# Performance work log

Hardware: AMD Instinct MI355X
Metric: run time of the kernel (lower is better)

The kernel has to match this reference:

```python
import jax, jax.numpy as jnp
import numpy as np


def setup_inputs() -> dict:
    key = jax.random.key(0)
    k0, k1, k2, k3 = jax.random.split(key, 4)
    H = 256  # hidden_dim_size
    DK = 256
    DV = 256
    hidden_states = jax.random.normal(k0, (1, 32, H, 16, 16), dtype=jnp.float32)
    # torch nn.Linear(H, dk, bias=False) computes x @ W.T; we store W.T directly as (H, dk)
    Wq = jax.random.normal(k1, (H, DK), dtype=jnp.float32) * (1.0 / np.sqrt(H))
    Wk = jax.random.normal(k2, (H, DK), dtype=jnp.float32) * (1.0 / np.sqrt(H))
    Wv = jax.random.normal(k3, (H, DV), dtype=jnp.float32) * (1.0 / np.sqrt(H))
    return {"hidden_states": hidden_states, "Wq": Wq, "Wk": Wk, "Wv": Wv}


def reference(hidden_states, Wq, Wk, Wv):
    # (b, t, c, h, w) -> (b, t, h, w, c)
    x = jnp.transpose(hidden_states, (0, 1, 3, 4, 2))
    nb, nt, nr, nc, nh = x.shape
    xf = x.reshape(-1, nh)  # (N, H) with N = b*t*h*w
    q = xf @ Wq             # (N, dk)
    k = xf @ Wk             # (N, dk)
    v = xf @ Wv             # (N, dv)
    dk = Wq.shape[1]
    scores = (q @ k.T) / jnp.sqrt(jnp.asarray(dk, dtype=q.dtype))  # (N, N)
    attn = jax.nn.softmax(scores, axis=-1) @ v                     # (N, dv)
    out = attn.reshape(nb, nt, nr, nc, -1)
    return jnp.transpose(out, (0, 1, 4, 2, 3))  # (b, t, dv, h, w)
```

## Files before the change

kernel.cpp:

```cpp
#include <hip/hip_runtime.h>
#include <stdint.h>

typedef __attribute__((ext_vector_type(8))) short bh8;
typedef __attribute__((ext_vector_type(4))) short bh4;
typedef __attribute__((ext_vector_type(4))) float f32x4;
typedef unsigned int uint32;

__device__ __forceinline__ unsigned short f2bf(float f) {
  uint32 u = __builtin_bit_cast(uint32, f);
  u += 0x7fffu + ((u >> 16) & 1u);
  return (unsigned short)(u >> 16);
}

__device__ __forceinline__ void lds_load16(const void* g, void* l) {
  auto gp = (const __attribute__((address_space(1))) uint32*)(uintptr_t)(g);
  auto lp = (__attribute__((address_space(3))) uint32*)(uintptr_t)(l);
  __builtin_amdgcn_global_load_lds(gp, lp, 16, 0, 0);
}

__global__ __launch_bounds__(256) void k_transpose(
    const float* __restrict__ hidden, const float* __restrict__ Wq,
    const float* __restrict__ Wk, const float* __restrict__ Wv,
    unsigned short* __restrict__ xb, unsigned short* __restrict__ wt) {
  int bid = blockIdx.x, c0 = blockIdx.y * 16, tid = threadIdx.x;
  const float* in; unsigned short* out; float scale = 1.0f;
  if (bid < 32) { in = hidden + (size_t)bid * 65536; out = xb + (size_t)bid * 65536; }
  else {
    int j = bid - 32;
    in = (j == 0) ? Wq : (j == 1 ? Wk : Wv);
    out = wt + (size_t)j * 65536;
    if (j == 0) scale = 0.0625f;
  }
  __shared__ uint32 lt[256 * 9];
  uint32 pk[8];
#pragma unroll
  for (int i = 0; i < 8; ++i) {
    float a = in[(size_t)(c0 + 2 * i) * 256 + tid] * scale;
    float b = in[(size_t)(c0 + 2 * i + 1) * 256 + tid] * scale;
    pk[i] = (uint32)f2bf(a) | ((uint32)f2bf(b) << 16);
  }
#pragma unroll
  for (int i = 0; i < 8; ++i) lt[tid * 9 + i] = pk[i];
  __syncthreads();
  int q2 = tid & 1;
#pragma unroll
  for (int rr = 0; rr < 2; ++rr) {
    int r = rr * 128 + (tid >> 1);
    uint4 v;
    v.x = lt[r * 9 + q2 * 4 + 0]; v.y = lt[r * 9 + q2 * 4 + 1];
    v.z = lt[r * 9 + q2 * 4 + 2]; v.w = lt[r * 9 + q2 * 4 + 3];
    *(uint4*)(out + (size_t)r * 256 + c0 + q2 * 8) = v;
  }
}

__global__ __launch_bounds__(256, 2) void k_gemm(
    const unsigned short* __restrict__ xb, const unsigned short* __restrict__ wt,
    unsigned short* __restrict__ qb, unsigned short* __restrict__ kb,
    unsigned short* __restrict__ vtb) {
  __shared__ char lds[32768];
  char* ldsA = lds; char* ldsB = lds + 16384;
  int tid = threadIdx.x, z = blockIdx.z;
  int l = tid & 63, w = tid >> 6, g = l >> 4, r15 = l & 15;
  int wr = w >> 1, wc = w & 1;
  const unsigned short *Ag, *Bg; unsigned short* out;
  int arow0, brow0; size_t ostride;
  if (z < 2) {
    Ag = xb; arow0 = blockIdx.x * 128;
    Bg = wt + (size_t)z * 65536; brow0 = blockIdx.y * 128;
    out = z ? kb : qb; ostride = 256;
  } else {
    Ag = wt + 2 * 65536; arow0 = blockIdx.y * 128;
    Bg = xb; brow0 = blockIdx.x * 128;
    out = vtb; ostride = 8192;
  }
  f32x4 acc[4][4];
#pragma unroll
  for (int i = 0; i < 4; ++i)
#pragma unroll
    for (int j = 0; j < 4; ++j) acc[i][j] = (f32x4){0.f, 0.f, 0.f, 0.f};

  for (int kk = 0; kk < 4; ++kk) {
    int c0 = kk * 64;
    __syncthreads();
#pragma unroll
    for (int p = 0; p < 4; ++p) {
      int off = p * 4096 + tid * 16;
      int row = off >> 7, ch = (off >> 4) & 7, sc = ch ^ (row & 7);
      lds_load16((const char*)Ag + ((size_t)(arow0 + row) * 256 + c0) * 2 + sc * 16, ldsA + off);
    }
#pragma unroll
    for (int p = 0; p < 4; ++p) {
      int off = p * 4096 + tid * 16;
      int row = off >> 7, ch = (off >> 4) & 7, sc = ch ^ (row & 7);
      lds_load16((const char*)Bg + ((size_t)(brow0 + row) * 256 + c0) * 2 + sc * 16, ldsB + off);
    }
    __syncthreads();
#pragma unroll
    for (int ks = 0; ks < 2; ++ks) {
      bh8 af[4], bfr[4];
#pragma unroll
      for (int i = 0; i < 4; ++i) {
        int rowa = wr * 64 + i * 16 + r15;
        af[i] = *(const bh8*)(ldsA + rowa * 128 + (((ks * 4 + g) ^ (rowa & 7)) * 16));
        int rowb = wc * 64 + i * 16 + r15;
        bfr[i] = *(const bh8*)(ldsB + rowb * 128 + (((ks * 4 + g) ^ (rowb & 7)) * 16));
      }
#pragma unroll
      for (int i = 0; i < 4; ++i)
#pragma unroll
        for (int j = 0; j < 4; ++j)
          acc[i][j] = __builtin_amdgcn_mfma_f32_16x16x32_bf16(af[i], bfr[j], acc[i][j], 0, 0, 0);
    }
  }
  __syncthreads();
#pragma unroll
  for (int i = 0; i < 4; ++i)
#pragma unroll
    for (int j = 0; j < 4; ++j)
#pragma unroll
      for (int r = 0; r < 4; ++r) {
        int rowl = wr * 64 + i * 16 + g * 4 + r;
        int coll = wc * 64 + j * 16 + r15;
        *(unsigned short*)(lds + rowl * 256 + coll * 2) = f2bf(acc[i][j][r]);
      }
  __syncthreads();
#pragma unroll
  for (int p = 0; p < 8; ++p) {
    int off = p * 4096 + tid * 16;
    int row = off >> 8, colb = off & 255;
    *(uint4*)((char*)out + ((size_t)(arow0 + row) * ostride + (size_t)brow0) * 2 + colb) =
        *(const uint4*)(lds + off);
  }
}

__global__ __launch_bounds__(512, 2) void k_attn(
    const unsigned short* __restrict__ qg, const unsigned short* __restrict__ kg,
    const unsigned short* __restrict__ vtg, float* __restrict__ Op,
    float* __restrict__ mp, float* __restrict__ lp, int S, int shift, int KS) {
  extern __shared__ char smem[];
  int tid = threadIdx.x;
  int w = tid >> 6, l = tid & 63, g = l >> 4, r15 = l & 15;
  char* Pl = smem + 131072 + w * 2176;
  int bid = blockIdx.x;
  int s = (bid >> 1) & (S - 1);
  int qb = ((bid >> (1 + shift)) << 1) | (bid & 1);
  int qrow0 = qb * 128 + w * 16;

  bh8 qf[8];
  const char* qrow = (const char*)qg + (size_t)(qrow0 + r15) * 512;
#pragma unroll
  for (int ds = 0; ds < 8; ++ds) qf[ds] = *(const bh8*)(qrow + ds * 64 + g * 16);
  asm volatile("s_waitcnt vmcnt(0)" ::: "memory");

  f32x4 o[16];
#pragma unroll
  for (int dt = 0; dt < 16; ++dt) o[dt] = (f32x4){0.f, 0.f, 0.f, 0.f};
  float m[4], ls[4];
#pragma unroll
  for (int r = 0; r < 4; ++r) { m[r] = -INFINITY; ls[r] = 0.f; }

  int nt = KS >> 6, kb0 = s * KS;

  auto stage = [&](int buf, int kvb) {
    char* Kd = smem + buf * 65536;
    char* Vd = Kd + 32768;
#pragma unroll
    for (int p = 0; p < 4; ++p) {
      int off = p * 8192 + tid * 16;
      int row = off >> 9, ch = (off >> 4) & 31;
      lds_load16((const char*)kg + (size_t)(kvb + row) * 512 + ((ch ^ (row & 7)) * 16), Kd + off);
    }
#pragma unroll
    for (int p = 0; p < 4; ++p) {
      int off = p * 8192 + tid * 16;
      int row = off >> 7, ch = (off >> 4) & 7;
      lds_load16((const char*)vtg + (size_t)row * 16384 + (size_t)kvb * 2 + ((ch ^ (row & 7)) * 16),
                 Vd + off);
    }
  };

  stage(0, kb0);

  for (int kt = 0; kt < nt; ++kt) {
    int cur = kt & 1;
    if (kt + 1 < nt) {
      stage(cur ^ 1, kb0 + (kt + 1) * 64);
      asm volatile("s_waitcnt vmcnt(8)" ::: "memory");
    } else {
      asm volatile("s_waitcnt vmcnt(0)" ::: "memory");
    }
    __builtin_amdgcn_s_barrier();
    char* Kl = smem + cur * 65536;
    char* Vl = Kl + 32768;

    f32x4 s4[4];
#pragma unroll
    for (int it = 0; it < 4; ++it) s4[it] = (f32x4){0.f, 0.f, 0.f, 0.f};
#pragma unroll
    for (int ds = 0; ds < 8; ++ds)
#pragma unroll
      for (int it = 0; it < 4; ++it) {
        int krow = it * 16 + r15;
        bh8 kf = *(const bh8*)(Kl + krow * 512 + (((ds * 4 + g) ^ (krow & 7)) * 16));
        s4[it] = __builtin_amdgcn_mfma_f32_16x16x32_bf16(qf[ds], kf, s4[it], 0, 0, 0);
      }

    float rmax[4];
#pragma unroll
    for (int r = 0; r < 4; ++r)
      rmax[r] = fmaxf(fmaxf(s4[0][r], s4[1][r]), fmaxf(s4[2][r], s4[3][r]));
#pragma unroll
    for (int d = 1; d < 16; d <<= 1)
#pragma unroll
      for (int r = 0; r < 4; ++r) rmax[r] = fmaxf(rmax[r], __shfl_xor(rmax[r], d));
    float scl[4];
#pragma unroll
    for (int r = 0; r < 4; ++r) {
      float mn = fmaxf(m[r], rmax[r]);
      scl[r] = __expf(m[r] - mn);
      m[r] = mn;
    }
    float rsum[4] = {0.f, 0.f, 0.f, 0.f};
#pragma unroll
    for (int it = 0; it < 4; ++it)
#pragma unroll
      for (int r = 0; r < 4; ++r) {
        float pv = __expf(s4[it][r] - m[r]);
        s4[it][r] = pv;
        rsum[r] += pv;
      }
#pragma unroll
    for (int d = 1; d < 16; d <<= 1)
#pragma unroll
      for (int r = 0; r < 4; ++r) rsum[r] += __shfl_xor(rsum[r], d);
    f32x4 sv = {scl[0], scl[1], scl[2], scl[3]};
#pragma unroll
    for (int r = 0; r < 4; ++r) ls[r] = ls[r] * scl[r] + rsum[r];
#pragma unroll
    for (int dt = 0; dt < 16; ++dt) o[dt] *= sv;

#pragma unroll
    for (int it = 0; it < 4; ++it)
#pragma unroll
      for (int r = 0; r < 4; ++r) {
        int prow = g * 4 + r;
        *(unsigned short*)(Pl + prow * 136 + (it * 16 + r15) * 2) = f2bf(s4[it][r]);
      }
    asm volatile("s_waitcnt lgkmcnt(0)" ::: "memory");
    bh8 pa[2];
#pragma unroll
    for (int ks = 0; ks < 2; ++ks) {
      const char* pb = Pl + r15 * 136 + ks * 64 + g * 16;
      bh4 lo = *(const bh4*)pb;
      bh4 hi = *(const bh4*)(pb + 8);
      bh8 t;
      t[0] = lo[0]; t[1] = lo[1]; t[2] = lo[2]; t[3] = lo[3];
      t[4] = hi[0]; t[5] = hi[1]; t[6] = hi[2]; t[7] = hi[3];
      pa[ks] = t;
    }
#pragma unroll
    for (int ks = 0; ks < 2; ++ks)
#pragma unroll
      for (int dt = 0; dt < 16; ++dt) {
        int vrow = dt * 16 + r15;
        bh8 vf = *(const bh8*)(Vl + vrow * 128 + (((ks * 4 + g) ^ (vrow & 7)) * 16));
        o[dt] = __builtin_amdgcn_mfma_f32_16x16x32_bf16(pa[ks], vf, o[dt], 0, 0, 0);
      }

    asm volatile("s_waitcnt lgkmcnt(0)" ::: "memory");
    __builtin_amdgcn_s_barrier();
  }

  int nrow = qrow0 + g * 4;
  float* ob = Op + ((size_t)s * 8192 + nrow) * 256 + r15;
#pragma unroll
  for (int r = 0; r < 4; ++r)
#pragma unroll
    for (int dt = 0; dt < 16; ++dt) ob[(size_t)r * 256 + dt * 16] = o[dt][r];
  if (r15 == 0) {
#pragma unroll
    for (int r = 0; r < 4; ++r) {
      mp[(size_t)s * 8192 + nrow + r] = m[r];
      lp[(size_t)s * 8192 + nrow + r] = ls[r];
    }
  }
}

__global__ __launch_bounds__(256) void k_combine(
    const float* __restrict__ Op, const float* __restrict__ mp,
    const float* __restrict__ lp, float* __restrict__ out, int S) {
  __shared__ float wsc[4 * 256];
  __shared__ float lt[32 * 257];
  int t = blockIdx.x, dc = blockIdx.y, tid = threadIdx.x;
  {
    int n = t * 256 + tid;
    float mt = -INFINITY;
#pragma unroll 4
    for (int s = 0; s < 4; ++s)
      if (s < S) mt = fmaxf(mt, mp[(size_t)s * 8192 + n]);
    float den = 0.f;
#pragma unroll 4
    for (int s = 0; s < 4; ++s)
      if (s < S) den += __expf(mp[(size_t)s * 8192 + n] - mt) * lp[(size_t)s * 8192 + n];
    float inv = 1.0f / den;
#pragma unroll 4
    for (int s = 0; s < 4; ++s)
      if (s < S) wsc[s * 256 + tid] = __expf(mp[(size_t)s * 8192 + n] - mt) * inv;
  }
  __syncthreads();
  int dl = tid & 31, pg8 = tid >> 5;
  for (int pg = 0; pg < 32; ++pg) {
    int p = pg * 8 + pg8;
    int n = t * 256 + p;
    float a = 0.f;
#pragma unroll 4
    for (int s = 0; s < 4; ++s)
      if (s < S) a += wsc[s * 256 + p] * Op[((size_t)s * 8192 + n) * 256 + dc * 32 + dl];
    lt[dl * 257 + p] = a;
  }
  __syncthreads();
  int d8 = tid >> 5, p0 = (tid & 31) * 8;
#pragma unroll
  for (int jj = 0; jj < 4; ++jj) {
    int dd = jj * 8 + d8;
    float4 v0, v1;
    v0.x = lt[dd * 257 + p0 + 0]; v0.y = lt[dd * 257 + p0 + 1];
    v0.z = lt[dd * 257 + p0 + 2]; v0.w = lt[dd * 257 + p0 + 3];
    v1.x = lt[dd * 257 + p0 + 4]; v1.y = lt[dd * 257 + p0 + 5];
    v1.z = lt[dd * 257 + p0 + 6]; v1.w = lt[dd * 257 + p0 + 7];
    float* ob = out + (size_t)t * 65536 + (size_t)(dc * 32 + dd) * 256 + p0;
    *(float4*)ob = v0;
    *(float4*)(ob + 4) = v1;
  }
}

extern "C" void kernel_launch(void* const* d_in, const int* in_sizes, int n_in,
                              void* d_out, int out_size, void* d_ws, size_t ws_size,
                              hipStream_t stream) {
  const float* hidden = (const float*)d_in[0];
  const float* Wq = (const float*)d_in[1];
  const float* Wk = (const float*)d_in[2];
  const float* Wv = (const float*)d_in[3];
  float* out = (float*)d_out;
  char* ws = (char*)d_ws;

  const size_t off_x  = 0;
  const size_t off_wt = 4ull << 20;
  const size_t off_q  = off_wt + 3ull * 131072;
  const size_t off_k  = off_q + 8192ull * 256 * 2;
  const size_t off_vt = off_k + 8192ull * 256 * 2;
  const size_t off_O  = off_vt + 8192ull * 256 * 2;

  int S = 4;
  {
    auto need = [&](int s) {
      return off_O + (size_t)s * 8192 * 256 * 4 + (size_t)s * 8192 * 4 * 2;
    };
    if (ws_size < need(4)) S = 2;
    if (ws_size < need(2)) S = 1;
  }
  size_t off_m = off_O + (size_t)S * 8192 * 256 * 4;
  size_t off_l = off_m + (size_t)S * 8192 * 4;

  unsigned short* xb  = (unsigned short*)(ws + off_x);
  unsigned short* wt  = (unsigned short*)(ws + off_wt);
  unsigned short* qb  = (unsigned short*)(ws + off_q);
  unsigned short* kb  = (unsigned short*)(ws + off_k);
  unsigned short* vtb = (unsigned short*)(ws + off_vt);
  float* Op = (float*)(ws + off_O);
  float* mp = (float*)(ws + off_m);
  float* lp = (float*)(ws + off_l);
  int shift = (S == 4) ? 2 : (S == 2 ? 1 : 0);
  int KS = 8192 / S;

  const int attn_lds = 131072 + 8 * 2176;
  hipFuncSetAttribute((const void*)k_attn, hipFuncAttributeMaxDynamicSharedMemorySize,
                      attn_lds);

  k_transpose<<<dim3(35, 16), dim3(256), 0, stream>>>(hidden, Wq, Wk, Wv, xb, wt);
  k_gemm<<<dim3(64, 2, 3), dim3(256), 0, stream>>>(xb, wt, qb, kb, vtb);
  k_attn<<<dim3(64 * S), dim3(512), attn_lds, stream>>>(qb, kb, vtb, Op, mp, lp, S, shift, KS);
  k_combine<<<dim3(32, 8), dim3(256), 0, stream>>>(Op, mp, lp, out, S);
}
```

Baseline: 173.5 us.

## Rework attention kernel to 32x32x16 MFMA with register-resident P operand

Rewrites the flash-attention kernel to use 32x32x16 bf16 MFMA with 4 waves each owning 32 query rows, computing S^T so each lane holds one query column. The P matrix is converted to bf16 with packed cvt instructions and reshuffled across lane halves with cross-lane shuffles, removing the LDS round-trip for P. Block size drops from 512 to 256 threads with one block per CU and the LDS scratch for P is removed. The larger tiles reduce LDS reads per FLOP and softmax reduction shuffles, at the cost of fewer resident waves and higher register pressure (16 q fragments plus 8 f32x16 accumulators).

```diff
diff --git a/kernel.cpp b/kernel.cpp
--- a/kernel.cpp
+++ b/kernel.cpp
@@ -2,14 +2,20 @@
 #include <stdint.h>
 
 typedef __attribute__((ext_vector_type(8))) short bh8;
-typedef __attribute__((ext_vector_type(4))) short bh4;
 typedef __attribute__((ext_vector_type(4))) float f32x4;
+typedef __attribute__((ext_vector_type(16))) float f32x16;
 typedef unsigned int uint32;
 
 __device__ __forceinline__ unsigned short f2bf(float f) {
   uint32 u = __builtin_bit_cast(uint32, f);
   u += 0x7fffu + ((u >> 16) & 1u);
   return (unsigned short)(u >> 16);
+}
+
+__device__ __forceinline__ uint32 cvtpk_bf16(float lo, float hi) {
+  uint32 r;
+  asm("v_cvt_pk_bf16_f32 %0, %1, %2" : "=v"(r) : "v"(lo), "v"(hi));
+  return r;
 }
 
 __device__ __forceinline__ void lds_load16(const void* g, void* l) {
@@ -133,31 +139,17 @@
   }
 }
 
-__global__ __launch_bounds__(512, 2) void k_attn(
+__global__ __launch_bounds__(256, 1) void k_attn(
     const unsigned short* __restrict__ qg, const unsigned short* __restrict__ kg,
     const unsigned short* __restrict__ vtg, float* __restrict__ Op,
     float* __restrict__ mp, float* __restrict__ lp, int S, int shift, int KS) {
   extern __shared__ char smem[];
   int tid = threadIdx.x;
-  int w = tid >> 6, l = tid & 63, g = l >> 4, r15 = l & 15;
-  char* Pl = smem + 131072 + w * 2176;
+  int w = tid >> 6, l = tid & 63, col = l & 31, half = l >> 5;
   int bid = blockIdx.x;
   int s = (bid >> 1) & (S - 1);
   int qb = ((bid >> (1 + shift)) << 1) | (bid & 1);
-  int qrow0 = qb * 128 + w * 16;
-
-  bh8 qf[8];
-  const char* qrow = (const char*)qg + (size_t)(qrow0 + r15) * 512;
-#pragma unroll
-  for (int ds = 0; ds < 8; ++ds) qf[ds] = *(const bh8*)(qrow + ds * 64 + g * 16);
-  asm volatile("s_waitcnt vmcnt(0)" ::: "memory");
-
-  f32x4 o[16];
-#pragma unroll
-  for (int dt = 0; dt < 16; ++dt) o[dt] = (f32x4){0.f, 0.f, 0.f, 0.f};
-  float m[4], ls[4];
-#pragma unroll
-  for (int r = 0; r < 4; ++r) { m[r] = -INFINITY; ls[r] = 0.f; }
+  int qrow0 = qb * 128 + w * 32;
 
   int nt = KS >> 6, kb0 = s * KS;
 
@@ -165,27 +157,41 @@
     char* Kd = smem + buf * 65536;
     char* Vd = Kd + 32768;
 #pragma unroll
-    for (int p = 0; p < 4; ++p) {
-      int off = p * 8192 + tid * 16;
+    for (int p = 0; p < 8; ++p) {
+      int off = p * 4096 + tid * 16;
       int row = off >> 9, ch = (off >> 4) & 31;
       lds_load16((const char*)kg + (size_t)(kvb + row) * 512 + ((ch ^ (row & 7)) * 16), Kd + off);
     }
 #pragma unroll
-    for (int p = 0; p < 4; ++p) {
-      int off = p * 8192 + tid * 16;
+    for (int p = 0; p < 8; ++p) {
+      int off = p * 4096 + tid * 16;
       int row = off >> 7, ch = (off >> 4) & 7;
       lds_load16((const char*)vtg + (size_t)row * 16384 + (size_t)kvb * 2 + ((ch ^ (row & 7)) * 16),
                  Vd + off);
     }
   };
 
+  bh8 qf[16];
+  {
+    const char* qrow = (const char*)qg + (size_t)(qrow0 + col) * 512 + half * 16;
+#pragma unroll
+    for (int t = 0; t < 16; ++t) qf[t] = *(const bh8*)(qrow + t * 32);
+  }
+
   stage(0, kb0);
+
+  f32x16 o[8];
+#pragma unroll
+  for (int dt = 0; dt < 8; ++dt)
+#pragma unroll
+    for (int i = 0; i < 16; ++i) o[dt][i] = 0.f;
+  float m = -INFINITY, ls = 0.f;
 
   for (int kt = 0; kt < nt; ++kt) {
     int cur = kt & 1;
     if (kt + 1 < nt) {
       stage(cur ^ 1, kb0 + (kt + 1) * 64);
-      asm volatile("s_waitcnt vmcnt(8)" ::: "memory");
+      asm volatile("s_waitcnt vmcnt(16)" ::: "memory");
     } else {
       asm volatile("s_waitcnt vmcnt(0)" ::: "memory");
     }
@@ -193,96 +199,89 @@
     char* Kl = smem + cur * 65536;
     char* Vl = Kl + 32768;
 
-    f32x4 s4[4];
-#pragma unroll
-    for (int it = 0; it < 4; ++it) s4[it] = (f32x4){0.f, 0.f, 0.f, 0.f};
-#pragma unroll
-    for (int ds = 0; ds < 8; ++ds)
-#pragma unroll
-      for (int it = 0; it < 4; ++it) {
-        int krow = it * 16 + r15;
-        bh8 kf = *(const bh8*)(Kl + krow * 512 + (((ds * 4 + g) ^ (krow & 7)) * 16));
-        s4[it] = __builtin_amdgcn_mfma_f32_16x16x32_bf16(qf[ds], kf, s4[it], 0, 0, 0);
+    f32x16 sc0, sc1;
+#pragma unroll
+    for (int i = 0; i < 16; ++i) { sc0[i] = 0.f; sc1[i] = 0.f; }
+#pragma unroll
+    for (int t = 0; t < 16; ++t) {
+      int r0 = col, r1 = 32 + col;
+      bh8 kf0 = *(const bh8*)(Kl + r0 * 512 + (((2 * t + half) ^ (r0 & 7)) * 16));
+      bh8 kf1 = *(const bh8*)(Kl + r1 * 512 + (((2 * t + half) ^ (r1 & 7)) * 16));
+      sc0 = __builtin_amdgcn_mfma_f32_32x32x16_bf16(kf0, qf[t], sc0, 0, 0, 0);
+      sc1 = __builtin_amdgcn_mfma_f32_32x32x16_bf16(kf1, qf[t], sc1, 0, 0, 0);
+    }
+
+    float rm = sc0[0];
+#pragma unroll
+    for (int i = 1; i < 16; ++i) rm = fmaxf(rm, sc0[i]);
+#pragma unroll
+    for (int i = 0; i < 16; ++i) rm = fmaxf(rm, sc1[i]);
+    rm = fmaxf(rm, __shfl_xor(rm, 32));
+    float mn = fmaxf(m, rm);
+    float scl = __expf(m - mn);
+    m = mn;
+    float rsum = 0.f;
+#pragma unroll
+    for (int i = 0; i < 16; ++i) { sc0[i] = __expf(sc0[i] - mn); rsum += sc0[i]; }
+#pragma unroll
+    for (int i = 0; i < 16; ++i) { sc1[i] = __expf(sc1[i] - mn); rsum += sc1[i]; }
+    rsum += __shfl_xor(rsum, 32);
+    ls = ls * scl + rsum;
+
+    float sclb[16];
+#pragma unroll
+    for (int i = 0; i < 16; ++i) {
+      int qs = (i & 3) + 8 * (i >> 2) + 4 * half;
+      sclb[i] = __shfl(scl, qs);
+    }
+#pragma unroll
+    for (int dt = 0; dt < 8; ++dt)
+#pragma unroll
+      for (int i = 0; i < 16; ++i) o[dt][i] *= sclb[i];
+
+    bh8 pa[4];
+#pragma unroll
+    for (int t2 = 0; t2 < 2; ++t2) {
+      const f32x16& p = t2 ? sc1 : sc0;
+      uint32 c0 = cvtpk_bf16(p[0], p[1]),  c1 = cvtpk_bf16(p[2], p[3]);
+      uint32 c2 = cvtpk_bf16(p[4], p[5]),  c3 = cvtpk_bf16(p[6], p[7]);
+      uint32 c4 = cvtpk_bf16(p[8], p[9]),  c5 = cvtpk_bf16(p[10], p[11]);
+      uint32 c6 = cvtpk_bf16(p[12], p[13]), c7 = cvtpk_bf16(p[14], p[15]);
+      uint32 za = half ? c0 : c2, zb = half ? c1 : c3;
+      uint32 zc = half ? c4 : c6, zd = half ? c5 : c7;
+      za = __shfl_xor((int)za, 32); zb = __shfl_xor((int)zb, 32);
+      zc = __shfl_xor((int)zc, 32); zd = __shfl_xor((int)zd, 32);
+      uint4 u0, u1;
+      if (half == 0) { u0 = (uint4){c0, c1, za, zb}; u1 = (uint4){c4, c5, zc, zd}; }
+      else           { u0 = (uint4){za, zb, c2, c3}; u1 = (uint4){zc, zd, c6, c7}; }
+      pa[2 * t2 + 0] = __builtin_bit_cast(bh8, u0);
+      pa[2 * t2 + 1] = __builtin_bit_cast(bh8, u1);
+    }
+
+#pragma unroll
+    for (int dt = 0; dt < 8; ++dt) {
+      int rv = dt * 32 + col;
+#pragma unroll
+      for (int ks = 0; ks < 4; ++ks) {
+        bh8 vf = *(const bh8*)(Vl + rv * 128 + (((2 * ks + half) ^ (rv & 7)) * 16));
+        o[dt] = __builtin_amdgcn_mfma_f32_32x32x16_bf16(pa[ks], vf, o[dt], 0, 0, 0);
       }
-
-    float rmax[4];
-#pragma unroll
-    for (int r = 0; r < 4; ++r)
-      rmax[r] = fmaxf(fmaxf(s4[0][r], s4[1][r]), fmaxf(s4[2][r], s4[3][r]));
-#pragma unroll
-    for (int d = 1; d < 16; d <<= 1)
-#pragma unroll
-      for (int r = 0; r < 4; ++r) rmax[r] = fmaxf(rmax[r], __shfl_xor(rmax[r], d));
-    float scl[4];
-#pragma unroll
-    for (int r = 0; r < 4; ++r) {
-      float mn = fmaxf(m[r], rmax[r]);
-      scl[r] = __expf(m[r] - mn);
-      m[r] = mn;
-    }
-    float rsum[4] = {0.f, 0.f, 0.f, 0.f};
-#pragma unroll
-    for (int it = 0; it < 4; ++it)
-#pragma unroll
-      for (int r = 0; r < 4; ++r) {
-        float pv = __expf(s4[it][r] - m[r]);
-        s4[it][r] = pv;
-        rsum[r] += pv;
-      }
-#pragma unroll
-    for (int d = 1; d < 16; d <<= 1)
-#pragma unroll
-      for (int r = 0; r < 4; ++r) rsum[r] += __shfl_xor(rsum[r], d);
-    f32x4 sv = {scl[0], scl[1], scl[2], scl[3]};
-#pragma unroll
-    for (int r = 0; r < 4; ++r) ls[r] = ls[r] * scl[r] + rsum[r];
-#pragma unroll
-    for (int dt = 0; dt < 16; ++dt) o[dt] *= sv;
-
-#pragma unroll
-    for (int it = 0; it < 4; ++it)
-#pragma unroll
-      for (int r = 0; r < 4; ++r) {
-        int prow = g * 4 + r;
-        *(unsigned short*)(Pl + prow * 136 + (it * 16 + r15) * 2) = f2bf(s4[it][r]);
-      }
-    asm volatile("s_waitcnt lgkmcnt(0)" ::: "memory");
-    bh8 pa[2];
-#pragma unroll
-    for (int ks = 0; ks < 2; ++ks) {
-      const char* pb = Pl + r15 * 136 + ks * 64 + g * 16;
-      bh4 lo = *(const bh4*)pb;
-      bh4 hi = *(const bh4*)(pb + 8);
-      bh8 t;
-      t[0] = lo[0]; t[1] = lo[1]; t[2] = lo[2]; t[3] = lo[3];
-      t[4] = hi[0]; t[5] = hi[1]; t[6] = hi[2]; t[7] = hi[3];
-      pa[ks] = t;
-    }
-#pragma unroll
-    for (int ks = 0; ks < 2; ++ks)
-#pragma unroll
-      for (int dt = 0; dt < 16; ++dt) {
-        int vrow = dt * 16 + r15;
-        bh8 vf = *(const bh8*)(Vl + vrow * 128 + (((ks * 4 + g) ^ (vrow & 7)) * 16));
-        o[dt] = __builtin_amdgcn_mfma_f32_16x16x32_bf16(pa[ks], vf, o[dt], 0, 0, 0);
-      }
+    }
 
     asm volatile("s_waitcnt lgkmcnt(0)" ::: "memory");
     __builtin_amdgcn_s_barrier();
   }
 
-  int nrow = qrow0 + g * 4;
-  float* ob = Op + ((size_t)s * 8192 + nrow) * 256 + r15;
-#pragma unroll
-  for (int r = 0; r < 4; ++r)
-#pragma unroll
-    for (int dt = 0; dt < 16; ++dt) ob[(size_t)r * 256 + dt * 16] = o[dt][r];
-  if (r15 == 0) {
-#pragma unroll
-    for (int r = 0; r < 4; ++r) {
-      mp[(size_t)s * 8192 + nrow + r] = m[r];
-      lp[(size_t)s * 8192 + nrow + r] = ls[r];
-    }
+#pragma unroll
+  for (int i = 0; i < 16; ++i) {
+    int qr = (i & 3) + 8 * (i >> 2) + 4 * half;
+    float* ob = Op + ((size_t)s * 8192 + qrow0 + qr) * 256 + col;
+#pragma unroll
+    for (int dt = 0; dt < 8; ++dt) ob[dt * 32] = o[dt][i];
+  }
+  if (l < 32) {
+    mp[(size_t)s * 8192 + qrow0 + col] = m;
+    lp[(size_t)s * 8192 + qrow0 + col] = ls;
   }
 }
 
@@ -373,12 +372,12 @@
   int shift = (S == 4) ? 2 : (S == 2 ? 1 : 0);
   int KS = 8192 / S;
 
-  const int attn_lds = 131072 + 8 * 2176;
+  const int attn_lds = 131072;
   hipFuncSetAttribute((const void*)k_attn, hipFuncAttributeMaxDynamicSharedMemorySize,
                       attn_lds);
 
   k_transpose<<<dim3(35, 16), dim3(256), 0, stream>>>(hidden, Wq, Wk, Wv, xb, wt);
   k_gemm<<<dim3(64, 2, 3), dim3(256), 0, stream>>>(xb, wt, qb, kb, vtb);
-  k_attn<<<dim3(64 * S), dim3(512), attn_lds, stream>>>(qb, kb, vtb, Op, mp, lp, S, shift, KS);
+  k_attn<<<dim3(64 * S), dim3(256), attn_lds, stream>>>(qb, kb, vtb, Op, mp, lp, S, shift, KS);
   k_combine<<<dim3(32, 8), dim3(256), 0, stream>>>(Op, mp, lp, out, S);
 }
```

Measured after the change: 184.6 us. +6.4%, slower.
